# Kernel tuning notes

Measured on AMD Instinct MI355X. Metric: run time of the kernel, lower is better.

## Reference

```python
import jax, jax.numpy as jnp
import numpy as np

K = 3  # kernel_size
S = 1  # stride
P = 1  # padding


def setup_inputs() -> dict:
    key = jax.random.key(0)
    ks = jax.random.split(key, 5)
    B, C, H, W, O = 4, 64, 128, 128, 64
    x = jax.random.normal(ks[0], (B, C, H, W), jnp.float32)
    # offset conv params (module inits these to 0; use small random values so the
    # bilinear-gather path is actually exercised with non-integer offsets)
    w_off = jax.random.normal(ks[1], (2 * K * K, C, K, K), jnp.float32) * 0.01
    b_off = jax.random.normal(ks[2], (2 * K * K,), jnp.float32) * 0.01
    # deformable conv params (torchvision DeformConv2d has bias=True by default)
    w_dcn = jax.random.normal(ks[3], (O, C, K, K), jnp.float32) * (1.0 / np.sqrt(C * K * K))
    b_dcn = jax.random.normal(ks[4], (O,), jnp.float32) * 0.01
    return {"x": x, "w_off": w_off, "b_off": b_off, "w_dcn": w_dcn, "b_dcn": b_dcn}


def _conv(x, w, b):
    y = jax.lax.conv_general_dilated(
        x, w, window_strides=(S, S), padding=[(P, P), (P, P)],
        dimension_numbers=("NCHW", "OIHW", "NCHW"))
    return y + b[None, :, None, None]


def _deform_conv2d(x, offset, w_dcn, b_dcn):
    # x: [B,C,H,W]; offset: [B, 2*K*K, Ho, Wo] with (dy, dx) interleaved per
    # kernel tap (row-major kh*K+kw), matching torchvision deform_conv2d.
    B, C, H, W = x.shape
    Ho, Wo = offset.shape[2], offset.shape[3]
    K2 = K * K
    off = offset.reshape(B, K2, 2, Ho, Wo)
    oy, ox = off[:, :, 0], off[:, :, 1]  # [B,K2,Ho,Wo]

    kh = (jnp.arange(K2) // K).astype(jnp.float32)
    kw = (jnp.arange(K2) % K).astype(jnp.float32)
    base_y = (jnp.arange(Ho) * S - P).astype(jnp.float32)
    base_x = (jnp.arange(Wo) * S - P).astype(jnp.float32)
    # fractional sampling locations: p0 + p_k + offset
    py = base_y[None, None, :, None] + kh[None, :, None, None] + oy  # [B,K2,Ho,Wo]
    px = base_x[None, None, None, :] + kw[None, :, None, None] + ox

    y0f = jnp.floor(py); x0f = jnp.floor(px)
    dy = py - y0f; dx = px - x0f
    y0 = y0f.astype(jnp.int32); x0 = x0f.astype(jnp.int32)

    def gather(yi, xi):
        # implicit zero padding: mask out-of-range corners
        valid = (yi >= 0) & (yi < H) & (xi >= 0) & (xi < W)
        yc = jnp.clip(yi, 0, H - 1)
        xc = jnp.clip(xi, 0, W - 1)
        v = jax.vmap(lambda xb, yb, xib: xb[:, yb, xib])(x, yc, xc)  # [B,C,K2,Ho,Wo]
        return v * valid[:, None].astype(x.dtype)

    v00 = gather(y0, x0)
    v01 = gather(y0, x0 + 1)
    v10 = gather(y0 + 1, x0)
    v11 = gather(y0 + 1, x0 + 1)

    wy = dy[:, None]; wx = dx[:, None]  # [B,1,K2,Ho,Wo]
    sampled = (v00 * (1 - wy) * (1 - wx) + v01 * (1 - wy) * wx
               + v10 * wy * (1 - wx) + v11 * wy * wx)  # [B,C,K2,Ho,Wo]

    O = w_dcn.shape[0]
    out = jnp.einsum("bckij,ock->boij", sampled, w_dcn.reshape(O, C, K2))
    return out + b_dcn[None, :, None, None]


def reference(x, w_off, b_off, w_dcn, b_dcn):
    offset = _conv(x, w_off, b_off)          # [B, 2*K*K, Ho, Wo]
    return _deform_conv2d(x, offset, w_dcn, b_dcn)
```

## Files before the change

kernel.cpp:

```cpp
#include <hip/hip_runtime.h>
#include <hip/hip_fp16.h>

#define B_ 4
#define H_ 128
#define W_ 128
#define HW_ 16384

typedef _Float16 half8 __attribute__((ext_vector_type(8)));
typedef float floatx16 __attribute__((ext_vector_type(16)));


__global__ __launch_bounds__(256) void k_prep_w(
    const float* __restrict__ w_dcn, const float* __restrict__ w_off,
    __half* __restrict__ W2L, __half* __restrict__ W0L)
{
    int idx = blockIdx.x*256 + threadIdx.x;
    if (idx < 36864) {
        int e = idx & 7, lane = (idx>>3) & 63, og = (idx>>9) & 1;
        int ks = (idx>>10) & 3, tap = idx >> 12;
        int o = og*32 + (lane & 31);
        int c = ks*16 + (lane >> 5)*8 + e;
        W2L[idx] = __float2half(w_dcn[o*576 + c*9 + tap]);
    } else {
        int i2 = idx - 36864;
        int e = i2 & 7, lane = (i2>>3) & 63;
        int ks = (i2>>9) & 3, tap = i2 >> 11;
        int oc = lane & 31;
        int c = ks*16 + (lane >> 5)*8 + e;
        W0L[i2] = (oc < 18) ? __float2half(w_off[oc*576 + c*9 + tap])
                            : __float2half(0.f);
    }
}

#define CHS2 3488
#define WLOC_OFF 27904
#define SMEM_SZ 37120

__global__ __launch_bounds__(128, 2) void k_fused(
    const float* __restrict__ x, const _Float16* __restrict__ W2L,
    const _Float16* __restrict__ W0L, const float* __restrict__ b_off,
    const float* __restrict__ b_dcn, float* __restrict__ out)
{
    __shared__ __attribute__((aligned(16))) char smem[SMEM_SZ];
    char* halo_c = smem;

    int t = threadIdx.x;
    int lane = t & 63;
    int v = __builtin_amdgcn_readfirstlane(t >> 6);
    int c31 = lane & 31;
    int h8  = lane >> 5;

    char*  wl   = smem + WLOC_OFF + v*4608;
    float* offL = (float*)wl;
    char*  desc = wl;

    int bid  = blockIdx.x;
    int xcd  = bid & 7, sidx = bid >> 3;
    int orig = xcd*128 + sidx;
    int b    = orig >> 8;
    int rem  = orig & 255;
    int i0   = (rem >> 2) * 2;
    int j0   = (rem & 3) * 32;

    const float* xf = x + (size_t)b * (64*HW_);

    for (int rep = 0; rep < 14; ++rep) {
        int idx = rep*128 + t;
        if (idx < 1728) {
            int ch = idx / 216, pl = idx - ch*216;
            int hr = pl / 36, hx = pl - hr*36;
            int grow = min(max(i0 - 2 + hr, 0), H_-1);
            int gcol = min(max(j0 - 2 + hx, 0), W_-1);
            int gpix = (grow<<7) + gcol;
            const float* s = xf + ch*8*HW_ + gpix;
            half8 vv;
            #pragma unroll
            for (int e = 0; e < 8; ++e) vv[e] = (_Float16)s[e*HW_];
            *(half8*)(halo_c + ch*CHS2 + pl*16) = vv;
        }
    }
    __syncthreads();

    floatx16 accA = {0.f,0.f,0.f,0.f,0.f,0.f,0.f,0.f,0.f,0.f,0.f,0.f,0.f,0.f,0.f,0.f};
    const half8 hz = {0,0,0,0,0,0,0,0};
    #pragma unroll
    for (int tap = 0; tap < 9; ++tap) {
        int kh = tap/3, kw = tap - (tap/3)*3;
        int ii = i0 + v - 1 + kh;
        int jj = j0 + c31 - 1 + kw;
        bool valid = (ii >= 0) && (ii < H_) && (jj >= 0) && (jj < W_);
        int pixA = (v + 1 + kh)*36 + (c31 + 1 + kw);
        #pragma unroll
        for (int s = 0; s < 4; ++s) {
            half8 a = *(const half8*)(halo_c + (s*2 + h8)*CHS2 + pixA*16);
            a = valid ? a : hz;
            half8 bf = *(const half8*)(W0L + ((tap*4+s)<<9) + (lane<<3));
            accA = __builtin_amdgcn_mfma_f32_32x32x16_f16(a, bf, accA, 0, 0, 0);
        }
    }
    {
        int oc = c31;
        if (oc < 18) {
            float bo = b_off[oc];
            #pragma unroll
            for (int r = 0; r < 16; ++r) {
                int row = (r & 3) + 8*(r >> 2) + 4*h8;
                offL[row*18 + oc] = accA[r] + bo;
            }
        }
    }

    float2 o2r[5];
    #pragma unroll
    for (int e = 0; e < 5; ++e) {
        int idx = e*64 + lane;
        if (idx < 288) {
            int pl = idx / 9, tap = idx - pl*9;
            o2r[e] = *(const float2*)(offL + pl*18 + 2*tap);
        }
    }
    uint4 dreg[5];
    #pragma unroll
    for (int e = 0; e < 5; ++e) {
        int idx = e*64 + lane;
        if (idx < 288) {
            int pl = idx / 9, tap = idx - pl*9;
            int kh = tap/3, kw = tap - (tap/3)*3;
            float py = (float)(i0 + v - 1 + kh) + o2r[e].x;
            float px = (float)(j0 + pl - 1 + kw) + o2r[e].y;
            float y0f = floorf(py), x0f = floorf(px);
            float dy = py - y0f, dx = px - x0f;
            int y0 = (int)y0f, x0i = (int)x0f;
            int y1 = y0 + 1,  x1 = x0i + 1;
            bool vy0 = (y0>=0)&(y0<H_),   vy1 = (y1>=0)&(y1<H_);
            bool vx0 = (x0i>=0)&(x0i<W_), vx1 = (x1>=0)&(x1<W_);
            int yc0 = min(max(y0,0),H_-1),  yc1 = min(max(y1,0),H_-1);
            int xc0 = min(max(x0i,0),W_-1), xc1 = min(max(x1,0),W_-1);
            float w00 = (1.f-dy)*(1.f-dx) * ((vy0&&vx0)?1.f:0.f);
            float w01 = (1.f-dy)*dx       * ((vy0&&vx1)?1.f:0.f);
            float w10 = dy*(1.f-dx)       * ((vy1&&vx0)?1.f:0.f);
            float w11 = dy*dx             * ((vy1&&vx1)?1.f:0.f);
            int hy0 = yc0 - (i0-2), hy1 = yc1 - (i0-2);
            int hx0 = xc0 - (j0-2), hx1 = xc1 - (j0-2);
            bool inh = ((unsigned)hy0 < 6u) & ((unsigned)hy1 < 6u)
                     & ((unsigned)hx0 < 36u) & ((unsigned)hx1 < 36u);
            unsigned a0,a1,a2,a3;
            if (inh) { a0 = hy0*36+hx0; a1 = hy0*36+hx1; a2 = hy1*36+hx0; a3 = hy1*36+hx1; }
            else     { a0 = ((yc0<<7)+xc0) | 0x8000u; a1 = (yc0<<7)+xc1;
                       a2 = (yc1<<7)+xc0;             a3 = (yc1<<7)+xc1; }
            __half2 hw0 = __floats2half2_rn(w00, w01);
            __half2 hw1 = __floats2half2_rn(w10, w11);
            dreg[e].x = a0 | (a1 << 16);
            dreg[e].y = a2 | (a3 << 16);
            dreg[e].z = *(unsigned*)&hw0;
            dreg[e].w = *(unsigned*)&hw1;
        }
    }
    #pragma unroll
    for (int e = 0; e < 5; ++e) {
        int idx = e*64 + lane;
        if (idx < 288) {
            int pl = idx / 9, tap = idx - pl*9;
            *(uint4*)(desc + (tap*32 + pl)*16) = dreg[e];
        }
    }

    floatx16 acc0 = {0.f,0.f,0.f,0.f,0.f,0.f,0.f,0.f,0.f,0.f,0.f,0.f,0.f,0.f,0.f,0.f};
    floatx16 acc1 = acc0;

    const char* hqs0 = halo_c + (0*2 + h8)*CHS2;
    const char* hqs1 = halo_c + (1*2 + h8)*CHS2;
    const char* hqs2 = halo_c + (2*2 + h8)*CHS2;
    const char* hqs3 = halo_c + (3*2 + h8)*CHS2;

    #pragma unroll 3
    for (int tap = 0; tap < 9; ++tap) {
        uint4 d = *(const uint4*)(desc + (tap*32 + c31)*16);
        unsigned p0i = d.x & 0x7fffu, p1i = d.x >> 16;
        unsigned p2i = d.y & 0xffffu, p3i = d.y >> 16;
        bool inh = (d.x & 0x8000u) == 0u;
        unsigned short b00 = (unsigned short)(d.z & 0xffffu);
        unsigned short b01 = (unsigned short)(d.z >> 16);
        unsigned short b10 = (unsigned short)(d.w & 0xffffu);
        unsigned short b11 = (unsigned short)(d.w >> 16);
        _Float16 h00 = *(_Float16*)&b00, h01 = *(_Float16*)&b01;
        _Float16 h10 = *(_Float16*)&b10, h11 = *(_Float16*)&b11;
        half8 W00 = {h00,h00,h00,h00,h00,h00,h00,h00};
        half8 W01 = {h01,h01,h01,h01,h01,h01,h01,h01};
        half8 W10 = {h10,h10,h10,h10,h10,h10,h10,h10};
        half8 W11 = {h11,h11,h11,h11,h11,h11,h11,h11};
        half8 sk[4];
        const char* hb[4] = {hqs0, hqs1, hqs2, hqs3};
        #pragma unroll
        for (int s = 0; s < 4; ++s) {
            half8 v00, v01, v10, v11;
            if (inh) {
                v00 = *(const half8*)(hb[s] + p0i*16);
                v01 = *(const half8*)(hb[s] + p1i*16);
                v10 = *(const half8*)(hb[s] + p2i*16);
                v11 = *(const half8*)(hb[s] + p3i*16);
            } else {
                int chb = (s*2 + h8)*8;
                #pragma unroll
                for (int e = 0; e < 8; ++e) {
                    v00[e] = (_Float16)xf[(chb+e)*HW_ + (int)p0i];
                    v01[e] = (_Float16)xf[(chb+e)*HW_ + (int)p1i];
                    v10[e] = (_Float16)xf[(chb+e)*HW_ + (int)p2i];
                    v11[e] = (_Float16)xf[(chb+e)*HW_ + (int)p3i];
                }
            }
            sk[s] = v00*W00 + v01*W01 + v10*W10 + v11*W11;
        }
        #pragma unroll
        for (int s = 0; s < 4; ++s) {
            half8 bf0 = *(const half8*)(W2L + (((tap*4+s)*2+0)<<9) + (lane<<3));
            acc0 = __builtin_amdgcn_mfma_f32_32x32x16_f16(sk[s], bf0, acc0, 0, 0, 0);
            half8 bf1 = *(const half8*)(W2L + (((tap*4+s)*2+1)<<9) + (lane<<3));
            acc1 = __builtin_amdgcn_mfma_f32_32x32x16_f16(sk[s], bf1, acc1, 0, 0, 0);
        }
    }
    __syncthreads();

    float* E = (float*)smem;
    #pragma unroll
    for (int r = 0; r < 16; ++r) {
        int row = (r & 3) + 8*(r >> 2) + 4*h8;
        int pl  = v*32 + row;
        E[pl*66 + c31]      = acc0[r];
        E[pl*66 + 32 + c31] = acc1[r];
    }
    __syncthreads();
    int obase = (b*64)*HW_ + i0*W_ + j0;
    int prow = (lane >> 5)*W_ + c31;
    #pragma unroll
    for (int rep = 0; rep < 32; ++rep) {
        int o = rep*2 + v;
        out[obase + o*HW_ + prow] = E[lane*66 + o] + b_dcn[o];
    }
}

extern "C" void kernel_launch(void* const* d_in, const int* in_sizes, int n_in,
                              void* d_out, int out_size, void* d_ws, size_t ws_size,
                              hipStream_t stream) {
    const float* x     = (const float*)d_in[0];
    const float* w_off = (const float*)d_in[1];
    const float* b_off = (const float*)d_in[2];
    const float* w_dcn = (const float*)d_in[3];
    const float* b_dcn = (const float*)d_in[4];
    float* out = (float*)d_out;

    __half* W2L = (__half*)d_ws;
    __half* W0L = (__half*)((char*)d_ws + 73728);

    k_prep_w<<<216, 256, 0, stream>>>(w_dcn, w_off, W2L, W0L);
    k_fused<<<1024, 128, 0, stream>>>(x, (const _Float16*)W2L,
                                      (const _Float16*)W0L, b_off, b_dcn, out);
}
```

Baseline: 93.38 us.

## Pre-convert input to channel-packed fp16 and stage halo via global_load_lds

A prep kernel now converts x to fp16 in an 8-channel-interleaved layout in workspace. The fused kernel then loads its halo tile with direct global-to-LDS 16-byte loads instead of eight strided fp32 loads and a conversion per element. The LDS channel stride drops its padding so the halo is contiguous, as the direct loads require. The cost is an extra full pass over x in the prep kernel plus an 8 MB fp16 write and read, and possible LDS bank conflicts now that the padding is gone.

```diff
diff --git a/kernel.cpp b/kernel.cpp
--- a/kernel.cpp
+++ b/kernel.cpp
@@ -8,38 +8,56 @@
 
 typedef _Float16 half8 __attribute__((ext_vector_type(8)));
 typedef float floatx16 __attribute__((ext_vector_type(16)));
-
-
-__global__ __launch_bounds__(256) void k_prep_w(
-    const float* __restrict__ w_dcn, const float* __restrict__ w_off,
-    __half* __restrict__ W2L, __half* __restrict__ W0L)
+typedef __attribute__((address_space(3))) void lds_void;
+typedef const __attribute__((address_space(1))) void gbl_void;
+
+
+__global__ __launch_bounds__(256) void k_prep(
+    const float* __restrict__ x, const float* __restrict__ w_dcn,
+    const float* __restrict__ w_off,
+    __half* __restrict__ W2L, __half* __restrict__ W0L,
+    _Float16* __restrict__ xh)
 {
-    int idx = blockIdx.x*256 + threadIdx.x;
-    if (idx < 36864) {
-        int e = idx & 7, lane = (idx>>3) & 63, og = (idx>>9) & 1;
-        int ks = (idx>>10) & 3, tap = idx >> 12;
-        int o = og*32 + (lane & 31);
-        int c = ks*16 + (lane >> 5)*8 + e;
-        W2L[idx] = __float2half(w_dcn[o*576 + c*9 + tap]);
+    int bid = blockIdx.x;
+    int t = threadIdx.x;
+    if (bid < 2048) {
+        int idx = bid*256 + t;
+        int p  = idx & (HW_-1);
+        int bc = idx >> 14;
+        const float* s = x + (size_t)bc*8*HW_ + p;
+        half8 vv;
+        #pragma unroll
+        for (int e = 0; e < 8; ++e) vv[e] = (_Float16)s[e*HW_];
+        *(half8*)(xh + (size_t)idx*8) = vv;
     } else {
-        int i2 = idx - 36864;
-        int e = i2 & 7, lane = (i2>>3) & 63;
-        int ks = (i2>>9) & 3, tap = i2 >> 11;
-        int oc = lane & 31;
-        int c = ks*16 + (lane >> 5)*8 + e;
-        W0L[i2] = (oc < 18) ? __float2half(w_off[oc*576 + c*9 + tap])
-                            : __float2half(0.f);
+        int idx = (bid - 2048)*256 + t;
+        if (idx < 36864) {
+            int e = idx & 7, lane = (idx>>3) & 63, og = (idx>>9) & 1;
+            int ks = (idx>>10) & 3, tap = idx >> 12;
+            int o = og*32 + (lane & 31);
+            int c = ks*16 + (lane >> 5)*8 + e;
+            W2L[idx] = __float2half(w_dcn[o*576 + c*9 + tap]);
+        } else {
+            int i2 = idx - 36864;
+            int e = i2 & 7, lane = (i2>>3) & 63;
+            int ks = (i2>>9) & 3, tap = i2 >> 11;
+            int oc = lane & 31;
+            int c = ks*16 + (lane >> 5)*8 + e;
+            W0L[i2] = (oc < 18) ? __float2half(w_off[oc*576 + c*9 + tap])
+                                : __float2half(0.f);
+        }
     }
 }
 
-#define CHS2 3488
-#define WLOC_OFF 27904
-#define SMEM_SZ 37120
+#define CHS2 3456
+#define WLOC_OFF 27648
+#define SMEM_SZ 36864
 
 __global__ __launch_bounds__(128, 2) void k_fused(
-    const float* __restrict__ x, const _Float16* __restrict__ W2L,
-    const _Float16* __restrict__ W0L, const float* __restrict__ b_off,
-    const float* __restrict__ b_dcn, float* __restrict__ out)
+    const float* __restrict__ x, const _Float16* __restrict__ xh,
+    const _Float16* __restrict__ W2L, const _Float16* __restrict__ W0L,
+    const float* __restrict__ b_off, const float* __restrict__ b_dcn,
+    float* __restrict__ out)
 {
     __shared__ __attribute__((aligned(16))) char smem[SMEM_SZ];
     char* halo_c = smem;
@@ -64,19 +82,23 @@
 
     const float* xf = x + (size_t)b * (64*HW_);
 
-    for (int rep = 0; rep < 14; ++rep) {
-        int idx = rep*128 + t;
-        if (idx < 1728) {
-            int ch = idx / 216, pl = idx - ch*216;
-            int hr = pl / 36, hx = pl - hr*36;
+    {
+        int nst  = 14 - v;
+        int base = v * 14;
+        const _Float16* xhb = xh + ((size_t)b << 20);
+        for (int s = 0; s < nst; ++s) {
+            int i   = base + s;
+            int idx = (i << 6) + lane;
+            int ch  = idx / 216;
+            int pl  = idx - ch*216;
+            int hr  = pl / 36;
+            int hx  = pl - hr*36;
             int grow = min(max(i0 - 2 + hr, 0), H_-1);
             int gcol = min(max(j0 - 2 + hx, 0), W_-1);
-            int gpix = (grow<<7) + gcol;
-            const float* s = xf + ch*8*HW_ + gpix;
-            half8 vv;
-            #pragma unroll
-            for (int e = 0; e < 8; ++e) vv[e] = (_Float16)s[e*HW_];
-            *(half8*)(halo_c + ch*CHS2 + pl*16) = vv;
+            const _Float16* g = xhb + ((size_t)ch << 17) + (size_t)(((grow<<7) + gcol) << 3);
+            __builtin_amdgcn_global_load_lds((gbl_void*)g,
+                                             (lds_void*)(halo_c + (i << 10)),
+                                             16, 0, 0);
         }
     }
     __syncthreads();
@@ -251,8 +273,9 @@
 
     __half* W2L = (__half*)d_ws;
     __half* W0L = (__half*)((char*)d_ws + 73728);
-
-    k_prep_w<<<216, 256, 0, stream>>>(w_dcn, w_off, W2L, W0L);
-    k_fused<<<1024, 128, 0, stream>>>(x, (const _Float16*)W2L,
+    _Float16* xh = (_Float16*)((char*)d_ws + 110592);
+
+    k_prep<<<2264, 256, 0, stream>>>(x, w_dcn, w_off, W2L, W0L, xh);
+    k_fused<<<1024, 128, 0, stream>>>(x, xh, (const _Float16*)W2L,
                                       (const _Float16*)W0L, b_off, b_dcn, out);
 }
```

Result: no change. 92.04 us (-1.4%).
